# Kernel tuning notes

Measured on AMD Instinct MI355X. Metric: run time of the kernel, lower is better.

Reference implementation:

```python
import jax, jax.numpy as jnp
import numpy as np

H, W = 48, 48
L = H * W            # 2304 tokens
D = 256              # d_model
NH = 8               # heads (self and memory attn)
FF = 1024            # dim_feedforward
T = 2                # memory frames
BS = 1
GN_GROUPS = 32       # GNActDWConv2d default groups


def layernorm(x, g, b, eps=1e-5):
    m = jnp.mean(x, -1, keepdims=True)
    v = jnp.mean((x - m) ** 2, -1, keepdims=True)
    return (x - m) * jax.lax.rsqrt(v + eps) * g + b


def linear(x, Wt, b):
    # torch nn.Linear convention: Wt is [out, in]
    return x @ Wt.T + b


def mha_core(Q, K, V, nhead):
    # Q [Lq, bs, C], K/V [Lk, bs, C]; AOT MultiheadAttention core (eval: no dropout)
    Lq, bs, C = Q.shape
    hd = C // nhead
    Qh = (Q / np.float32(np.sqrt(hd))).reshape(Lq, bs, nhead, hd).transpose(1, 2, 0, 3)
    Kh = K.reshape(-1, bs, nhead, hd).transpose(1, 2, 0, 3)
    Vh = V.reshape(-1, bs, nhead, hd).transpose(1, 2, 0, 3)
    attn = jax.nn.softmax(jnp.einsum('bhqd,bhkd->bhqk', Qh, Kh), axis=-1)
    out = jnp.einsum('bhqk,bhkd->bhqd', attn, Vh)
    return out.transpose(2, 0, 1, 3).reshape(Lq, bs, C)


def groupnorm(x, g, b, groups, eps=1e-5):
    bs, c, h, w = x.shape
    xg = x.reshape(bs, groups, c // groups, h, w)
    m = jnp.mean(xg, (2, 3, 4), keepdims=True)
    v = jnp.mean((xg - m) ** 2, (2, 3, 4), keepdims=True)
    xg = (xg - m) * jax.lax.rsqrt(v + eps)
    return xg.reshape(bs, c, h, w) * g[None, :, None, None] + b[None, :, None, None]


def dwconv5(x, k):
    # depthwise 5x5, padding=2; x [bs,c,h,w], k [c,1,5,5]
    return jax.lax.conv_general_dilated(x, k, (1, 1), ((2, 2), (2, 2)),
                                        feature_group_count=x.shape[1])


def setup_inputs() -> dict:
    key = jax.random.key(0)
    ks = jax.random.split(key, 16)
    rn = lambda i, shape, s=1.0: jax.random.normal(ks[i], shape, jnp.float32) * s
    w = 0.02
    inp = {
        'tgt': rn(0, (L, BS, D)),
        'global_K': rn(1, (T, L, BS, D)),
        'global_V': rn(2, (T, L, BS, D)),
        'local_K': rn(3, (L, BS, D)),
        'local_V': rn(4, (L, BS, D)),
        # LayerNorms
        'ln1_g': jnp.ones(D, jnp.float32), 'ln1_b': jnp.zeros(D, jnp.float32),
        'ln2_g': jnp.ones(D, jnp.float32), 'ln2_b': jnp.zeros(D, jnp.float32),
        'ln3_g': jnp.ones(D, jnp.float32), 'ln3_b': jnp.zeros(D, jnp.float32),
        'ln4_g': jnp.ones(D, jnp.float32), 'ln4_b': jnp.zeros(D, jnp.float32),
        # self_attn (use_linear=True) Q/K/V + projection
        'sa_Wq': rn(5, (D, D), w), 'sa_bq': jnp.zeros(D, jnp.float32),
        'sa_Wk': rn(6, (D, D), w), 'sa_bk': jnp.zeros(D, jnp.float32),
        'sa_Wv': rn(7, (D, D), w), 'sa_bv': jnp.zeros(D, jnp.float32),
        'sa_Wo': rn(8, (D, D), w), 'sa_bo': jnp.zeros(D, jnp.float32),
        # block linear_Q
        'Wq': rn(9, (D, D), w), 'bq': jnp.zeros(D, jnp.float32),
        # long/short term attn projections (use_linear=False)
        'lt_Wo': rn(10, (D, D), w), 'lt_bo': jnp.zeros(D, jnp.float32),
        'st_Wo': rn(11, (D, D), w), 'st_bo': jnp.zeros(D, jnp.float32),
        # FFN: linear1 -> GN+GELU+DWConv -> linear2
        'W1': rn(12, (FF, D), w), 'b1': jnp.zeros(FF, jnp.float32),
        'gn_g': jnp.ones(FF, jnp.float32), 'gn_b': jnp.zeros(FF, jnp.float32),
        'dw_k': rn(13, (FF, 1, 5, 5), 0.05),
        'W2': rn(14, (D, FF), w), 'b2': jnp.zeros(D, jnp.float32),
    }
    return inp


def reference(tgt, global_K, global_V, local_K, local_V,
              ln1_g, ln1_b, ln2_g, ln2_b, ln3_g, ln3_b, ln4_g, ln4_b,
              sa_Wq, sa_bq, sa_Wk, sa_bk, sa_Wv, sa_bv, sa_Wo, sa_bo,
              Wq, bq, lt_Wo, lt_bo, st_Wo, st_bo,
              W1, b1, gn_g, gn_b, dw_k, W2, b2):
    # --- stage 1: self-attention ---
    _tgt = layernorm(tgt, ln1_g, ln1_b)
    q = linear(_tgt, sa_Wq, sa_bq)
    k = linear(_tgt, sa_Wk, sa_bk)
    v = linear(_tgt, sa_Wv, sa_bv)
    tgt2 = linear(mha_core(q, k, v, NH), sa_Wo, sa_bo)
    tgt = tgt + tgt2  # droppath is identity at eval

    # --- stage 2: long-term + short-term memory cross-attention ---
    _tgt = layernorm(tgt, ln2_g, ln2_b)
    curr_Q = linear(_tgt, Wq, bq)
    curr_K = curr_Q
    curr_V = _tgt

    flat_K = global_K.reshape(-1, BS, D)  # [T*L, bs, D]
    flat_V = global_V.reshape(-1, BS, D)
    tgt2 = linear(mha_core(curr_Q, flat_K, flat_V, NH), lt_Wo, lt_bo)

    k_st = layernorm(local_K + curr_K, ln4_g, ln4_b)
    v_st = layernorm(local_V + curr_V, ln4_g, ln4_b)
    tgt3 = linear(mha_core(curr_Q, k_st, v_st, NH), st_Wo, st_bo)

    tgt = tgt + tgt2 + tgt3

    # --- stage 3: FFN with GN + GELU + depthwise conv ---
    _tgt = layernorm(tgt, ln3_g, ln3_b)
    x = linear(_tgt, W1, b1)                        # [L, bs, FF]
    x = x.reshape(H, W, BS, FF).transpose(2, 3, 0, 1)  # [bs, FF, H, W]
    x = jax.nn.gelu(groupnorm(x, gn_g, gn_b, GN_GROUPS), approximate=False)
    x = dwconv5(x, dw_k)
    x = x.reshape(BS, FF, L).transpose(2, 0, 1)     # [L, bs, FF]
    tgt2 = linear(x, W2, b2)
    return tgt + tgt2
```

## Files before the change

kernel.cpp:

```cpp
#include <hip/hip_runtime.h>
#include <hip/hip_bf16.h>

#define L   2304
#define D   256
#define NHD 8
#define HD  32
#define FF  1024
#define HH  48
#define WWW 48
#define SPL 4
#define RCH 24
#define RP  (L / RCH)
#define S2LOG 0.25503486f

typedef unsigned short bfraw;
typedef __attribute__((ext_vector_type(8))) short s8v;
typedef __attribute__((ext_vector_type(4))) float f4v;

__device__ __forceinline__ bfraw f2b(float x) {
    __hip_bfloat16 h = __float2bfloat16(x);
    return __builtin_bit_cast(bfraw, h);
}

__global__ __launch_bounds__(256) void diag_kernel(float* __restrict__ out, float c, int n)
{
    int i = blockIdx.x * 256 + threadIdx.x;
    if (i < n) out[i] = c;
}

__global__ __launch_bounds__(256) void ln_kernel(
    const float* __restrict__ inA, const float* __restrict__ inB,
    const float* __restrict__ g, const float* __restrict__ b,
    float* __restrict__ out, bfraw* __restrict__ outb)
{
    int row = blockIdx.x, t = threadIdx.x;
    size_t idx = (size_t)row * D + t;
    float v = inA[idx];
    if (inB) v += inB[idx];
    __shared__ float rs[256], rq[256];
    rs[t] = v; rq[t] = v * v;
    __syncthreads();
    for (int o = 128; o > 0; o >>= 1) {
        if (t < o) { rs[t] += rs[t + o]; rq[t] += rq[t + o]; }
        __syncthreads();
    }
    float mean = rs[0] * (1.f / D);
    float var  = rq[0] * (1.f / D) - mean * mean;
    float rstd = rsqrtf(var + 1e-5f);
    float r = (v - mean) * rstd * g[t] + b[t];
    out[idx] = r;
    if (outb) outb[idx] = f2b(r);
}

__global__ __launch_bounds__(256) void gemm_mfma(
    const float* __restrict__ A, const float* __restrict__ W,
    const float* __restrict__ bias, const float* res, float* out,
    bfraw* __restrict__ outb, float oscale,
    int M, int N, int K)
{
    __shared__ __attribute__((aligned(16))) short Al[32][32];
    __shared__ __attribute__((aligned(16))) short Wl[64][32];
    int t = threadIdx.x;
    int w = t >> 6, l = t & 63;
    int lo = l & 15, quad = l >> 4;
    int m0 = blockIdx.x * 32, n0 = blockIdx.y * 64;
    int wr = (w & 1) * 16, wc = (w >> 1) * 32;
    f4v acc[2];
    acc[0] = (f4v){0.f, 0.f, 0.f, 0.f};
    acc[1] = (f4v){0.f, 0.f, 0.f, 0.f};

    int aswz = (quad ^ ((lo >> 2) & 3)) * 8;
    int arow = t >> 3, apart = t & 7;
    int acol = ((apart >> 1) ^ ((arow >> 2) & 3)) * 8 + (apart & 1) * 4;

    for (int k0 = 0; k0 < K; k0 += 32) {
        float4 a4 = *reinterpret_cast<const float4*>(A + (size_t)(m0 + arow) * K + k0 + apart * 4);
        float4 w4[2];
        #pragma unroll
        for (int i = 0; i < 2; i++) {
            int row = i * 32 + arow;
            w4[i] = *reinterpret_cast<const float4*>(W + (size_t)(n0 + row) * K + k0 + apart * 4);
        }
        __syncthreads();
        {
            ushort4 ab;
            ab.x = f2b(a4.x); ab.y = f2b(a4.y); ab.z = f2b(a4.z); ab.w = f2b(a4.w);
            *reinterpret_cast<ushort4*>(&Al[arow][acol]) = ab;
            #pragma unroll
            for (int i = 0; i < 2; i++) {
                int row = i * 32 + arow;
                int col = ((apart >> 1) ^ ((row >> 2) & 3)) * 8 + (apart & 1) * 4;
                ushort4 wb;
                wb.x = f2b(w4[i].x); wb.y = f2b(w4[i].y); wb.z = f2b(w4[i].z); wb.w = f2b(w4[i].w);
                *reinterpret_cast<ushort4*>(&Wl[row][col]) = wb;
            }
        }
        __syncthreads();
        s8v af = *reinterpret_cast<const s8v*>(&Al[wr + lo][aswz]);
        #pragma unroll
        for (int j = 0; j < 2; j++) {
            s8v wf = *reinterpret_cast<const s8v*>(&Wl[wc + j * 16 + lo][aswz]);
            acc[j] = __builtin_amdgcn_mfma_f32_16x16x32_bf16(af, wf, acc[j], 0, 0, 0);
        }
    }

    #pragma unroll
    for (int j = 0; j < 2; j++) {
        #pragma unroll
        for (int r = 0; r < 4; r++) {
            int mrow = m0 + wr + quad * 4 + r;
            int ncol = n0 + wc + j * 16 + lo;
            float v = acc[j][r] + bias[ncol];
            size_t idx = (size_t)mrow * N + ncol;
            if (res) v += res[idx];
            out[idx] = v;
            if (outb) outb[idx] = f2b(v * oscale);
        }
    }
}

__global__ __launch_bounds__(256) void cvt_kernel(
    const float* __restrict__ in, bfraw* __restrict__ out)
{
    size_t i = ((size_t)blockIdx.x * 256 + threadIdx.x) * 4;
    float4 v = *reinterpret_cast<const float4*>(in + i);
    ushort4 o;
    o.x = f2b(v.x); o.y = f2b(v.y); o.z = f2b(v.z); o.w = f2b(v.w);
    *reinterpret_cast<ushort4*>(out + i) = o;
}

__global__ __launch_bounds__(256) void cvtT_kernel(
    const float* __restrict__ in, bfraw* __restrict__ out, int N)
{
    __shared__ float Ls[32][33];
    int h = blockIdx.y, n0 = blockIdx.x * 32, t = threadIdx.x;
    int nl = t >> 3, dq = t & 7;
    float4 v = *reinterpret_cast<const float4*>(in + (size_t)(n0 + nl) * D + h * HD + dq * 4);
    Ls[nl][dq*4+0] = v.x; Ls[nl][dq*4+1] = v.y;
    Ls[nl][dq*4+2] = v.z; Ls[nl][dq*4+3] = v.w;
    __syncthreads();
    int dl = t >> 3, nq = t & 7;
    ushort4 o;
    o.x = f2b(Ls[nq*4+0][dl]); o.y = f2b(Ls[nq*4+1][dl]);
    o.z = f2b(Ls[nq*4+2][dl]); o.w = f2b(Ls[nq*4+3][dl]);
    *reinterpret_cast<ushort4*>(out + (size_t)(h * HD + dl) * N + n0 + nq * 4) = o;
}

__global__ __launch_bounds__(256) void attn_mfma_split(
    const bfraw* __restrict__ Qb, const bfraw* __restrict__ Kb,
    const bfraw* __restrict__ Vt, float* __restrict__ OP,
    float* __restrict__ ML, int Lk, int chunk)
{
    __shared__ __attribute__((aligned(16))) short Ks[64][32];
    __shared__ __attribute__((aligned(16))) short Vts[32][72];
    __shared__ __attribute__((aligned(16))) short Ps[4][16][72];
    __shared__ float Tb[4][16][33];
    int t = threadIdx.x;
    int w = t >> 6, l = t & 63;
    int h = blockIdx.y, q0 = blockIdx.x * 64 + w * 16, z = blockIdx.z;
    int lo = l & 15, quad = l >> 4;
    int kb = z * chunk, ke = kb + chunk;

    s8v qf = *reinterpret_cast<const s8v*>(Qb + (size_t)(q0 + lo) * D + h * HD + quad * 8);
    int kswz = (quad ^ ((lo >> 2) & 3)) * 8;

    int skey = t >> 2, spart = t & 3;
    int kcol = (spart ^ ((skey >> 2) & 3)) * 8;
    int sd = t >> 3, svp = t & 7;
    const bfraw* kp = Kb + (size_t)skey * D + h * HD + spart * 8;
    const bfraw* vp = Vt + (size_t)(h * HD + sd) * Lk + svp * 8;

    float m_r = -1e30f, l_r = 0.f;
    f4v o0 = {0.f, 0.f, 0.f, 0.f}, o1 = {0.f, 0.f, 0.f, 0.f};

    for (int k0 = kb; k0 < ke; k0 += 64) {
        s8v kv = *reinterpret_cast<const s8v*>(kp + (size_t)k0 * D);
        s8v vv = *reinterpret_cast<const s8v*>(vp + k0);
        __syncthreads();
        *reinterpret_cast<s8v*>(&Ks[skey][kcol]) = kv;
        *reinterpret_cast<s8v*>(&Vts[sd][svp * 8]) = vv;
        __syncthreads();

        f4v sc4[4];
        #pragma unroll
        for (int s = 0; s < 4; s++) {
            s8v kf = *reinterpret_cast<const s8v*>(&Ks[lo + 16 * s][kswz]);
            sc4[s] = __builtin_amdgcn_mfma_f32_16x16x32_bf16(kf, qf, (f4v){0.f,0.f,0.f,0.f}, 0, 0, 0);
        }
        float cm = -1e30f;
        #pragma unroll
        for (int s = 0; s < 4; s++)
            #pragma unroll
            for (int r = 0; r < 4; r++)
                cm = fmaxf(cm, sc4[s][r]);
        cm = fmaxf(cm, __shfl_xor(cm, 16));
        cm = fmaxf(cm, __shfl_xor(cm, 32));
        bool skip = __all(cm <= m_r + 8.f);
        if (!skip) {
            float mnew = fmaxf(m_r, cm);
            float alpha = __builtin_amdgcn_exp2f(m_r - mnew);
            l_r *= alpha;
            #pragma unroll
            for (int r = 0; r < 4; r++) { o0[r] *= alpha; o1[r] *= alpha; }
            m_r = mnew;
        }
        float ls = 0.f;
        #pragma unroll
        for (int s = 0; s < 4; s++) {
            float p0 = __builtin_amdgcn_exp2f(sc4[s][0] - m_r);
            float p1 = __builtin_amdgcn_exp2f(sc4[s][1] - m_r);
            float p2 = __builtin_amdgcn_exp2f(sc4[s][2] - m_r);
            float p3 = __builtin_amdgcn_exp2f(sc4[s][3] - m_r);
            ls += p0 + p1 + p2 + p3;
            ushort4 pk;
            pk.x = f2b(p0); pk.y = f2b(p1); pk.z = f2b(p2); pk.w = f2b(p3);
            *reinterpret_cast<ushort4*>(&Ps[w][lo][s * 16 + quad * 4]) = pk;
        }
        ls += __shfl_xor(ls, 16);
        ls += __shfl_xor(ls, 32);
        l_r += ls;
        #pragma unroll
        for (int kc = 0; kc < 2; kc++) {
            s8v pf = *reinterpret_cast<const s8v*>(&Ps[w][lo][kc * 32 + quad * 8]);
            s8v v0 = *reinterpret_cast<const s8v*>(&Vts[lo][kc * 32 + quad * 8]);
            s8v v1 = *reinterpret_cast<const s8v*>(&Vts[16 + lo][kc * 32 + quad * 8]);
            o0 = __builtin_amdgcn_mfma_f32_16x16x32_bf16(v0, pf, o0, 0, 0, 0);
            o1 = __builtin_amdgcn_mfma_f32_16x16x32_bf16(v1, pf, o1, 0, 0, 0);
        }
    }

    #pragma unroll
    for (int r = 0; r < 4; r++) {
        Tb[w][lo][quad * 4 + r]      = o0[r];
        Tb[w][lo][16 + quad * 4 + r] = o1[r];
    }
    float* Oz = OP + (size_t)z * L * D;
    int ql = l >> 2, dq = (l & 3) * 8;
    float4 u0, u1;
    u0.x = Tb[w][ql][dq + 0]; u0.y = Tb[w][ql][dq + 1];
    u0.z = Tb[w][ql][dq + 2]; u0.w = Tb[w][ql][dq + 3];
    u1.x = Tb[w][ql][dq + 4]; u1.y = Tb[w][ql][dq + 5];
    u1.z = Tb[w][ql][dq + 6]; u1.w = Tb[w][ql][dq + 7];
    *reinterpret_cast<float4*>(Oz + (size_t)(q0 + ql) * D + h * HD + dq)     = u0;
    *reinterpret_cast<float4*>(Oz + (size_t)(q0 + ql) * D + h * HD + dq + 4) = u1;
    if (l < 16) {
        size_t mi = (((size_t)z * NHD + h) * L + q0 + lo) * 2;
        ML[mi]     = m_r;
        ML[mi + 1] = l_r;
    }
}

__global__ __launch_bounds__(256) void attn_combine(
    const float* __restrict__ OP, const float* __restrict__ ML,
    float* __restrict__ O)
{
    int q = blockIdx.x, t = threadIdx.x, h = t >> 5;
    float m[SPL], lv[SPL];
    float M = -1e30f;
    #pragma unroll
    for (int s = 0; s < SPL; s++) {
        size_t mi = (((size_t)s * NHD + h) * L + q) * 2;
        m[s]  = ML[mi];
        lv[s] = ML[mi + 1];
        M = fmaxf(M, m[s]);
    }
    float wl = 0.f, acc = 0.f;
    #pragma unroll
    for (int s = 0; s < SPL; s++) {
        float w = __builtin_amdgcn_exp2f(m[s] - M);
        wl  += w * lv[s];
        acc += w * OP[(size_t)s * L * D + (size_t)q * D + t];
    }
    O[(size_t)q * D + t] = acc / wl;
}

__global__ __launch_bounds__(256) void gn_stats_part(
    const float* __restrict__ X, float* __restrict__ ps)
{
    int g = blockIdx.x, rc = blockIdx.y, t = threadIdx.x;
    int cq = (t & 7) * 4;
    int rl = t >> 3;
    int r0 = rc * RP;
    float s = 0.f, sq = 0.f;
    #pragma unroll
    for (int p = 0; p < RP / 32; p++) {
        int l = r0 + p * 32 + rl;
        float4 v = *reinterpret_cast<const float4*>(X + (size_t)l * FF + g * 32 + cq);
        s  += v.x + v.y + v.z + v.w;
        sq += v.x*v.x + v.y*v.y + v.z*v.z + v.w*v.w;
    }
    __shared__ float rs[256], rq[256];
    rs[t] = s; rq[t] = sq;
    __syncthreads();
    for (int o = 128; o > 0; o >>= 1) {
        if (t < o) { rs[t] += rs[t + o]; rq[t] += rq[t + o]; }
        __syncthreads();
    }
    if (t == 0) {
        ps[(g * RCH + rc) * 2]     = rs[0];
        ps[(g * RCH + rc) * 2 + 1] = rq[0];
    }
}

__global__ __launch_bounds__(64) void gn_stats_final(
    const float* __restrict__ ps, float* __restrict__ st)
{
    int g = threadIdx.x;
    if (g < 32) {
        float s = 0.f, sq = 0.f;
        for (int i = 0; i < RCH; i++) {
            s  += ps[(g * RCH + i) * 2];
            sq += ps[(g * RCH + i) * 2 + 1];
        }
        float n = (float)(L * 32);
        float mean = s / n;
        float var  = sq / n - mean * mean;
        st[g * 2]     = mean;
        st[g * 2 + 1] = rsqrtf(var + 1e-5f);
    }
}

__global__ __launch_bounds__(256) void gn_gelu_dwconv(
    const float* __restrict__ X, const float* __restrict__ st,
    const float* __restrict__ gg, const float* __restrict__ gb,
    const float* __restrict__ Kw, float* __restrict__ Y)
{
    __shared__ float tile[144][64];
    int h0 = blockIdx.x * 8, w0 = blockIdx.y * 8, c0 = blockIdx.z * 64;
    int t = threadIdx.x;
    int c = t & 63;
    int cg = (c0 + c) >> 5;
    float mu = st[2 * cg], rs = st[2 * cg + 1];
    float ga = gg[c0 + c], be = gb[c0 + c];

    for (int i = t; i < 144 * 64; i += 256) {
        int sp = i >> 6;
        int hy = h0 + (sp / 12) - 2, wx = w0 + (sp % 12) - 2;
        float v = 0.f;
        if (hy >= 0 && hy < HH && wx >= 0 && wx < WWW) {
            float x = X[(size_t)(hy * WWW + wx) * FF + c0 + c];
            x = (x - mu) * rs * ga + be;
            v = 0.5f * x * (1.f + erff(x * 0.70710678118654752f));
        }
        tile[sp][c] = v;
    }
    float kw[25];
    #pragma unroll
    for (int i = 0; i < 25; i++) kw[i] = Kw[(size_t)(c0 + c) * 25 + i];
    __syncthreads();

    int sgrp = t >> 6;
    for (int s = 0; s < 16; s++) {
        int sp = sgrp * 16 + s;
        int oh = sp >> 3, ow = sp & 7;
        float acc = 0.f;
        #pragma unroll
        for (int ky = 0; ky < 5; ky++)
            #pragma unroll
            for (int kx = 0; kx < 5; kx++)
                acc += tile[(oh + ky) * 12 + ow + kx][c] * kw[ky * 5 + kx];
        Y[(size_t)((h0 + oh) * WWW + w0 + ow) * FF + c0 + c] = acc;
    }
}

extern "C" void kernel_launch(void* const* d_in, const int* in_sizes, int n_in,
                              void* d_out, int out_size, void* d_ws, size_t ws_size,
                              hipStream_t stream)
{
    (void)in_sizes;
    float* out = (float*)d_out;

    if (n_in != 34) {
        diag_kernel<<<(out_size + 255) / 256, 256, 0, stream>>>(out, 2000.f, out_size);
        return;
    }

    const float* tgt    = (const float*)d_in[0];
    const float* gK     = (const float*)d_in[1];
    const float* gV     = (const float*)d_in[2];
    const float* lK     = (const float*)d_in[3];
    const float* lV     = (const float*)d_in[4];
    const float* ln1_g  = (const float*)d_in[5];
    const float* ln1_b  = (const float*)d_in[6];
    const float* ln2_g  = (const float*)d_in[7];
    const float* ln2_b  = (const float*)d_in[8];
    const float* ln3_g  = (const float*)d_in[9];
    const float* ln3_b  = (const float*)d_in[10];
    const float* ln4_g  = (const float*)d_in[11];
    const float* ln4_b  = (const float*)d_in[12];
    const float* sa_Wq  = (const float*)d_in[13];
    const float* sa_bq  = (const float*)d_in[14];
    const float* sa_Wk  = (const float*)d_in[15];
    const float* sa_bk  = (const float*)d_in[16];
    const float* sa_Wv  = (const float*)d_in[17];
    const float* sa_bv  = (const float*)d_in[18];
    const float* sa_Wo  = (const float*)d_in[19];
    const float* sa_bo  = (const float*)d_in[20];
    const float* Wq     = (const float*)d_in[21];
    const float* bq     = (const float*)d_in[22];
    const float* lt_Wo  = (const float*)d_in[23];
    const float* lt_bo  = (const float*)d_in[24];
    const float* st_Wo  = (const float*)d_in[25];
    const float* st_bo  = (const float*)d_in[26];
    const float* W1w    = (const float*)d_in[27];
    const float* b1w    = (const float*)d_in[28];
    const float* gn_g   = (const float*)d_in[29];
    const float* gn_b   = (const float*)d_in[30];
    const float* dw_k   = (const float*)d_in[31];
    const float* W2w    = (const float*)d_in[32];
    const float* b2w    = (const float*)d_in[33];

    const size_t LD = (size_t)L * D;
    const size_t NEED = (6 * LD + (size_t)L * FF + 64) * 4;
    float* ws = (float*)d_ws;
    float* t0 = ws + 0 * LD;
    float* t1 = ws + 1 * LD;
    float* t2 = ws + 2 * LD;
    float* t3 = ws + 3 * LD;
    float* t4 = ws + 4 * LD;
    float* t5 = ws + 5 * LD;
    float* X1 = t0;
    float* X2 = ws + 6 * LD;
    float* ST = X2 + (size_t)L * FF;
    bfraw* qb   = (bfraw*)X2;
    bfraw* kb1  = qb + LD;
    bfraw* vtb1 = qb + 3 * LD;
    bfraw* kb2  = qb + 5 * LD;
    bfraw* vtb2 = qb + 6 * LD;
    float* OP   = ws;
    float* ML   = X2 + (7 * LD) / 2;
    float* PS   = ML;

    if (ws_size < NEED) {
        int wsMiB = (int)(ws_size >> 20); if (wsMiB > 63) wsMiB = 63;
        diag_kernel<<<(out_size + 255) / 256, 256, 0, stream>>>(out, 64.f + (float)wsMiB, out_size);
        return;
    }

    dim3 gDD(L / 32, D / 64);
    dim3 gDF(L / 32, FF / 64);
    dim3 gATS(L / 64, NHD, SPL);
    int  cvtLD  = (int)(LD / 1024);
    dim3 gT1(L / 32, NHD);
    dim3 gT2(2 * L / 32, NHD);
    dim3 gGN(32, RCH);
    dim3 gDW(6, 6, 16);

    ln_kernel<<<L, 256, 0, stream>>>(tgt, nullptr, ln1_g, ln1_b, t0, nullptr);
    gemm_mfma<<<gDD, 256, 0, stream>>>(t0, sa_Wq, sa_bq, nullptr, t1, qb,  S2LOG, L, D, D);
    gemm_mfma<<<gDD, 256, 0, stream>>>(t0, sa_Wk, sa_bk, nullptr, t2, kb2, 1.f,   L, D, D);
    gemm_mfma<<<gDD, 256, 0, stream>>>(t0, sa_Wv, sa_bv, nullptr, t3, nullptr, 1.f, L, D, D);
    cvtT_kernel<<<gT1, 256, 0, stream>>>(t3, vtb2, L);
    attn_mfma_split<<<gATS, 256, 0, stream>>>(qb, kb2, vtb2, OP, ML, L, L / SPL);
    attn_combine<<<L, 256, 0, stream>>>(OP, ML, t4);
    gemm_mfma<<<gDD, 256, 0, stream>>>(t4, sa_Wo, sa_bo, tgt, t5, nullptr, 1.f, L, D, D);

    ln_kernel<<<L, 256, 0, stream>>>(t5, nullptr, ln2_g, ln2_b, t0, nullptr);
    gemm_mfma<<<gDD, 256, 0, stream>>>(t0, Wq, bq, nullptr, t1, qb, S2LOG, L, D, D);
    ln_kernel<<<L, 256, 0, stream>>>(t1, lK, ln4_g, ln4_b, t2, kb2);
    ln_kernel<<<L, 256, 0, stream>>>(t0, lV, ln4_g, ln4_b, t3, nullptr);
    cvtT_kernel<<<gT1, 256, 0, stream>>>(t3, vtb2, L);
    cvt_kernel<<<2 * cvtLD, 256, 0, stream>>>(gK, kb1);
    cvtT_kernel<<<gT2, 256, 0, stream>>>(gV, vtb1, 2 * L);
    attn_mfma_split<<<gATS, 256, 0, stream>>>(qb, kb1, vtb1, OP, ML, 2 * L, 2 * L / SPL);
    attn_combine<<<L, 256, 0, stream>>>(OP, ML, t4);
    gemm_mfma<<<gDD, 256, 0, stream>>>(t4, lt_Wo, lt_bo, t5, t5, nullptr, 1.f, L, D, D);
    attn_mfma_split<<<gATS, 256, 0, stream>>>(qb, kb2, vtb2, OP, ML, L, L / SPL);
    attn_combine<<<L, 256, 0, stream>>>(OP, ML, t4);
    gemm_mfma<<<gDD, 256, 0, stream>>>(t4, st_Wo, st_bo, t5, t5, nullptr, 1.f, L, D, D);

    ln_kernel<<<L, 256, 0, stream>>>(t5, nullptr, ln3_g, ln3_b, t4, nullptr);
    gemm_mfma<<<gDF, 256, 0, stream>>>(t4, W1w, b1w, nullptr, X1, nullptr, 1.f, L, FF, D);
    gn_stats_part<<<gGN, 256, 0, stream>>>(X1, PS);
    gn_stats_final<<<1, 64, 0, stream>>>(PS, ST);
    gn_gelu_dwconv<<<gDW, 256, 0, stream>>>(X1, ST, gn_g, gn_b, dw_k, X2);
    gemm_mfma<<<gDD, 256, 0, stream>>>(X2, W2w, b2w, t5, out, nullptr, 1.f, L, D, FF);
}
```

Before: 348.3 us.

## Fuse self-attention QKV projections into one GEMM and restructure GEMM staging

Replaces the three separate Q/K/V projection GEMMs plus the V transpose-convert kernel with a single fused kernel that selects the weight by grid row and writes bf16 Q (scaled), K, and transposed V directly. It also restructures the general GEMM so that a 256-wide K chunk of the weight is staged in shared memory with an XOR swizzle, while the A operand is read straight from global memory into registers. The aim is fewer launches, fewer fp32 intermediate writes and fewer syncs per K step. The trade-off is a larger shared-memory footprint, which may lower occupancy, plus uncoalesced A loads and strided transposed V stores.

```diff
diff --git a/kernel.cpp b/kernel.cpp
--- a/kernel.cpp
+++ b/kernel.cpp
@@ -58,8 +58,7 @@
     bfraw* __restrict__ outb, float oscale,
     int M, int N, int K)
 {
-    __shared__ __attribute__((aligned(16))) short Al[32][32];
-    __shared__ __attribute__((aligned(16))) short Wl[64][32];
+    __shared__ __attribute__((aligned(16))) short Wl[64][256];
     int t = threadIdx.x;
     int w = t >> 6, l = t & 63;
     int lo = l & 15, quad = l >> 4;
@@ -69,38 +68,39 @@
     acc[0] = (f4v){0.f, 0.f, 0.f, 0.f};
     acc[1] = (f4v){0.f, 0.f, 0.f, 0.f};
 
-    int aswz = (quad ^ ((lo >> 2) & 3)) * 8;
-    int arow = t >> 3, apart = t & 7;
-    int acol = ((apart >> 1) ^ ((arow >> 2) & 3)) * 8 + (apart & 1) * 4;
-
-    for (int k0 = 0; k0 < K; k0 += 32) {
-        float4 a4 = *reinterpret_cast<const float4*>(A + (size_t)(m0 + arow) * K + k0 + apart * 4);
-        float4 w4[2];
-        #pragma unroll
-        for (int i = 0; i < 2; i++) {
-            int row = i * 32 + arow;
-            w4[i] = *reinterpret_cast<const float4*>(W + (size_t)(n0 + row) * K + k0 + apart * 4);
-        }
+    int srow = t >> 2, scolq = t & 3;
+    const float* wp = W + (size_t)(n0 + srow) * K + scolq * 64;
+    const float* ap = A + (size_t)(m0 + wr + lo) * K + quad * 8;
+
+    for (int ch = 0; ch < K; ch += 256) {
         __syncthreads();
-        {
-            ushort4 ab;
-            ab.x = f2b(a4.x); ab.y = f2b(a4.y); ab.z = f2b(a4.z); ab.w = f2b(a4.w);
-            *reinterpret_cast<ushort4*>(&Al[arow][acol]) = ab;
+        #pragma unroll
+        for (int i = 0; i < 8; i++) {
+            float4 x = *reinterpret_cast<const float4*>(wp + ch + i * 8);
+            float4 y = *reinterpret_cast<const float4*>(wp + ch + i * 8 + 4);
+            s8v wb;
+            wb[0] = (short)f2b(x.x); wb[1] = (short)f2b(x.y);
+            wb[2] = (short)f2b(x.z); wb[3] = (short)f2b(x.w);
+            wb[4] = (short)f2b(y.x); wb[5] = (short)f2b(y.y);
+            wb[6] = (short)f2b(y.z); wb[7] = (short)f2b(y.w);
+            *reinterpret_cast<s8v*>(&Wl[srow][((scolq * 8 + i) ^ (srow & 7)) * 8]) = wb;
+        }
+        __syncthreads();
+        #pragma unroll
+        for (int kk = 0; kk < 8; kk++) {
+            float4 a0 = *reinterpret_cast<const float4*>(ap + ch + kk * 32);
+            float4 a1 = *reinterpret_cast<const float4*>(ap + ch + kk * 32 + 4);
+            s8v af;
+            af[0] = (short)f2b(a0.x); af[1] = (short)f2b(a0.y);
+            af[2] = (short)f2b(a0.z); af[3] = (short)f2b(a0.w);
+            af[4] = (short)f2b(a1.x); af[5] = (short)f2b(a1.y);
+            af[6] = (short)f2b(a1.z); af[7] = (short)f2b(a1.w);
             #pragma unroll
-            for (int i = 0; i < 2; i++) {
-                int row = i * 32 + arow;
-                int col = ((apart >> 1) ^ ((row >> 2) & 3)) * 8 + (apart & 1) * 4;
-                ushort4 wb;
-                wb.x = f2b(w4[i].x); wb.y = f2b(w4[i].y); wb.z = f2b(w4[i].z); wb.w = f2b(w4[i].w);
-                *reinterpret_cast<ushort4*>(&Wl[row][col]) = wb;
+            for (int j = 0; j < 2; j++) {
+                int rw = wc + j * 16 + lo;
+                s8v wf = *reinterpret_cast<const s8v*>(&Wl[rw][((kk * 4 + quad) ^ (rw & 7)) * 8]);
+                acc[j] = __builtin_amdgcn_mfma_f32_16x16x32_bf16(af, wf, acc[j], 0, 0, 0);
             }
-        }
-        __syncthreads();
-        s8v af = *reinterpret_cast<const s8v*>(&Al[wr + lo][aswz]);
-        #pragma unroll
-        for (int j = 0; j < 2; j++) {
-            s8v wf = *reinterpret_cast<const s8v*>(&Wl[wc + j * 16 + lo][aswz]);
-            acc[j] = __builtin_amdgcn_mfma_f32_16x16x32_bf16(af, wf, acc[j], 0, 0, 0);
         }
     }
 
@@ -113,8 +113,79 @@
             float v = acc[j][r] + bias[ncol];
             size_t idx = (size_t)mrow * N + ncol;
             if (res) v += res[idx];
-            out[idx] = v;
+            if (out) out[idx] = v;
             if (outb) outb[idx] = f2b(v * oscale);
+        }
+    }
+}
+
+__global__ __launch_bounds__(256) void gemm_qkv(
+    const float* __restrict__ A,
+    const float* __restrict__ Wq_, const float* __restrict__ bq_,
+    const float* __restrict__ Wk_, const float* __restrict__ bk_,
+    const float* __restrict__ Wv_, const float* __restrict__ bv_,
+    bfraw* __restrict__ qb, bfraw* __restrict__ kb, bfraw* __restrict__ vtb)
+{
+    __shared__ __attribute__((aligned(16))) short Wl[64][256];
+    int t = threadIdx.x;
+    int w = t >> 6, l = t & 63;
+    int lo = l & 15, quad = l >> 4;
+    int sel = blockIdx.y >> 2;
+    int m0 = blockIdx.x * 32, n0 = (blockIdx.y & 3) * 64;
+    int wr = (w & 1) * 16, wc = (w >> 1) * 32;
+    const float* W = (sel == 0) ? Wq_ : (sel == 1) ? Wk_ : Wv_;
+    const float* bias = (sel == 0) ? bq_ : (sel == 1) ? bk_ : bv_;
+    f4v acc[2];
+    acc[0] = (f4v){0.f, 0.f, 0.f, 0.f};
+    acc[1] = (f4v){0.f, 0.f, 0.f, 0.f};
+
+    int srow = t >> 2, scolq = t & 3;
+    const float* wp = W + (size_t)(n0 + srow) * D + scolq * 64;
+    const float* ap = A + (size_t)(m0 + wr + lo) * D + quad * 8;
+
+    #pragma unroll
+    for (int i = 0; i < 8; i++) {
+        float4 x = *reinterpret_cast<const float4*>(wp + i * 8);
+        float4 y = *reinterpret_cast<const float4*>(wp + i * 8 + 4);
+        s8v wb;
+        wb[0] = (short)f2b(x.x); wb[1] = (short)f2b(x.y);
+        wb[2] = (short)f2b(x.z); wb[3] = (short)f2b(x.w);
+        wb[4] = (short)f2b(y.x); wb[5] = (short)f2b(y.y);
+        wb[6] = (short)f2b(y.z); wb[7] = (short)f2b(y.w);
+        *reinterpret_cast<s8v*>(&Wl[srow][((scolq * 8 + i) ^ (srow & 7)) * 8]) = wb;
+    }
+    __syncthreads();
+    #pragma unroll
+    for (int kk = 0; kk < 8; kk++) {
+        float4 a0 = *reinterpret_cast<const float4*>(ap + kk * 32);
+        float4 a1 = *reinterpret_cast<const float4*>(ap + kk * 32 + 4);
+        s8v af;
+        af[0] = (short)f2b(a0.x); af[1] = (short)f2b(a0.y);
+        af[2] = (short)f2b(a0.z); af[3] = (short)f2b(a0.w);
+        af[4] = (short)f2b(a1.x); af[5] = (short)f2b(a1.y);
+        af[6] = (short)f2b(a1.z); af[7] = (short)f2b(a1.w);
+        #pragma unroll
+        for (int j = 0; j < 2; j++) {
+            int rw = wc + j * 16 + lo;
+            s8v wf = *reinterpret_cast<const s8v*>(&Wl[rw][((kk * 4 + quad) ^ (rw & 7)) * 8]);
+            acc[j] = __builtin_amdgcn_mfma_f32_16x16x32_bf16(af, wf, acc[j], 0, 0, 0);
+        }
+    }
+
+    #pragma unroll
+    for (int j = 0; j < 2; j++) {
+        #pragma unroll
+        for (int r = 0; r < 4; r++) {
+            int mrow = m0 + wr + quad * 4 + r;
+            int ncol = n0 + wc + j * 16 + lo;
+            float v = acc[j][r] + bias[ncol];
+            if (sel == 0) {
+                qb[(size_t)mrow * D + ncol] = f2b(v * S2LOG);
+            } else if (sel == 1) {
+                kb[(size_t)mrow * D + ncol] = f2b(v);
+            } else {
+                vtb[(size_t)ncol * L + mrow] = f2b(v);
+            }
         }
     }
 }
@@ -439,6 +510,7 @@
 
     dim3 gDD(L / 32, D / 64);
     dim3 gDF(L / 32, FF / 64);
+    dim3 gQKV(L / 32, 12);
     dim3 gATS(L / 64, NHD, SPL);
     int  cvtLD  = (int)(LD / 1024);
     dim3 gT1(L / 32, NHD);
@@ -447,10 +519,8 @@
     dim3 gDW(6, 6, 16);
 
     ln_kernel<<<L, 256, 0, stream>>>(tgt, nullptr, ln1_g, ln1_b, t0, nullptr);
-    gemm_mfma<<<gDD, 256, 0, stream>>>(t0, sa_Wq, sa_bq, nullptr, t1, qb,  S2LOG, L, D, D);
-    gemm_mfma<<<gDD, 256, 0, stream>>>(t0, sa_Wk, sa_bk, nullptr, t2, kb2, 1.f,   L, D, D);
-    gemm_mfma<<<gDD, 256, 0, stream>>>(t0, sa_Wv, sa_bv, nullptr, t3, nullptr, 1.f, L, D, D);
-    cvtT_kernel<<<gT1, 256, 0, stream>>>(t3, vtb2, L);
+    gemm_qkv<<<gQKV, 256, 0, stream>>>(t0, sa_Wq, sa_bq, sa_Wk, sa_bk, sa_Wv, sa_bv,
+                                       qb, kb2, vtb2);
     attn_mfma_split<<<gATS, 256, 0, stream>>>(qb, kb2, vtb2, OP, ML, L, L / SPL);
     attn_combine<<<L, 256, 0, stream>>>(OP, ML, t4);
     gemm_mfma<<<gDD, 256, 0, stream>>>(t4, sa_Wo, sa_bo, tgt, t5, nullptr, 1.f, L, D, D);
```

After: 387.9 us. 11.4% more time.

## Feed GEMM A operand as bf16 directly from producers, skip LDS staging

Applied to the files above, without the earlier changes.

Producers of GEMM inputs (layernorm, attention combine, GN+GELU+dwconv) now write bf16, and the GEMM loads its A fragments straight from global memory into registers instead of converting fp32 to bf16 through shared memory. Unused fp32 outputs are dropped via null pointers. This halves A-operand traffic, removes one LDS staging buffer and the conversion work per tile, and cuts redundant fp32 stores. The tradeoff is uncoalesced per-lane 16-byte global loads for A. Precision is unchanged because the values were already rounded to bf16 before the MFMA.

```diff
diff --git a/kernel.cpp b/kernel.cpp
--- a/kernel.cpp
+++ b/kernel.cpp
@@ -48,17 +48,16 @@
     float var  = rq[0] * (1.f / D) - mean * mean;
     float rstd = rsqrtf(var + 1e-5f);
     float r = (v - mean) * rstd * g[t] + b[t];
-    out[idx] = r;
+    if (out)  out[idx]  = r;
     if (outb) outb[idx] = f2b(r);
 }
 
 __global__ __launch_bounds__(256) void gemm_mfma(
-    const float* __restrict__ A, const float* __restrict__ W,
+    const bfraw* __restrict__ A, const float* __restrict__ W,
     const float* __restrict__ bias, const float* res, float* out,
     bfraw* __restrict__ outb, float oscale,
     int M, int N, int K)
 {
-    __shared__ __attribute__((aligned(16))) short Al[32][32];
     __shared__ __attribute__((aligned(16))) short Wl[64][32];
     int t = threadIdx.x;
     int w = t >> 6, l = t & 63;
@@ -70,36 +69,29 @@
     acc[1] = (f4v){0.f, 0.f, 0.f, 0.f};
 
     int aswz = (quad ^ ((lo >> 2) & 3)) * 8;
-    int arow = t >> 3, apart = t & 7;
-    int acol = ((apart >> 1) ^ ((arow >> 2) & 3)) * 8 + (apart & 1) * 4;
+    int srow = t >> 3, spart = t & 7;
+    const bfraw* ap = A + (size_t)(m0 + wr + lo) * K + quad * 8;
 
     for (int k0 = 0; k0 < K; k0 += 32) {
-        float4 a4 = *reinterpret_cast<const float4*>(A + (size_t)(m0 + arow) * K + k0 + apart * 4);
         float4 w4[2];
         #pragma unroll
+        for (int i = 0; i < 2; i++)
+            w4[i] = *reinterpret_cast<const float4*>(W + (size_t)(n0 + i * 32 + srow) * K + k0 + spart * 4);
+        s8v af = *reinterpret_cast<const s8v*>(ap + k0);
+        __syncthreads();
+        #pragma unroll
         for (int i = 0; i < 2; i++) {
-            int row = i * 32 + arow;
-            w4[i] = *reinterpret_cast<const float4*>(W + (size_t)(n0 + row) * K + k0 + apart * 4);
-        }
-        __syncthreads();
-        {
-            ushort4 ab;
-            ab.x = f2b(a4.x); ab.y = f2b(a4.y); ab.z = f2b(a4.z); ab.w = f2b(a4.w);
-            *reinterpret_cast<ushort4*>(&Al[arow][acol]) = ab;
-            #pragma unroll
-            for (int i = 0; i < 2; i++) {
-                int row = i * 32 + arow;
-                int col = ((apart >> 1) ^ ((row >> 2) & 3)) * 8 + (apart & 1) * 4;
-                ushort4 wb;
-                wb.x = f2b(w4[i].x); wb.y = f2b(w4[i].y); wb.z = f2b(w4[i].z); wb.w = f2b(w4[i].w);
-                *reinterpret_cast<ushort4*>(&Wl[row][col]) = wb;
-            }
-        }
-        __syncthreads();
-        s8v af = *reinterpret_cast<const s8v*>(&Al[wr + lo][aswz]);
+            int row = i * 32 + srow;
+            int col = ((spart >> 1) ^ ((row >> 2) & 3)) * 8 + (spart & 1) * 4;
+            ushort4 wb;
+            wb.x = f2b(w4[i].x); wb.y = f2b(w4[i].y); wb.z = f2b(w4[i].z); wb.w = f2b(w4[i].w);
+            *reinterpret_cast<ushort4*>(&Wl[row][col]) = wb;
+        }
+        __syncthreads();
         #pragma unroll
         for (int j = 0; j < 2; j++) {
-            s8v wf = *reinterpret_cast<const s8v*>(&Wl[wc + j * 16 + lo][aswz]);
+            int rw = wc + j * 16 + lo;
+            s8v wf = *reinterpret_cast<const s8v*>(&Wl[rw][aswz]);
             acc[j] = __builtin_amdgcn_mfma_f32_16x16x32_bf16(af, wf, acc[j], 0, 0, 0);
         }
     }
@@ -113,7 +105,7 @@
             float v = acc[j][r] + bias[ncol];
             size_t idx = (size_t)mrow * N + ncol;
             if (res) v += res[idx];
-            out[idx] = v;
+            if (out) out[idx] = v;
             if (outb) outb[idx] = f2b(v * oscale);
         }
     }
@@ -252,7 +244,7 @@
 
 __global__ __launch_bounds__(256) void attn_combine(
     const float* __restrict__ OP, const float* __restrict__ ML,
-    float* __restrict__ O)
+    bfraw* __restrict__ Ob)
 {
     int q = blockIdx.x, t = threadIdx.x, h = t >> 5;
     float m[SPL], lv[SPL];
@@ -271,7 +263,7 @@
         wl  += w * lv[s];
         acc += w * OP[(size_t)s * L * D + (size_t)q * D + t];
     }
-    O[(size_t)q * D + t] = acc / wl;
+    Ob[(size_t)q * D + t] = f2b(acc / wl);
 }
 
 __global__ __launch_bounds__(256) void gn_stats_part(
@@ -323,7 +315,7 @@
 __global__ __launch_bounds__(256) void gn_gelu_dwconv(
     const float* __restrict__ X, const float* __restrict__ st,
     const float* __restrict__ gg, const float* __restrict__ gb,
-    const float* __restrict__ Kw, float* __restrict__ Y)
+    const float* __restrict__ Kw, bfraw* __restrict__ Y)
 {
     __shared__ float tile[144][64];
     int h0 = blockIdx.x * 8, w0 = blockIdx.y * 8, c0 = blockIdx.z * 64;
@@ -359,7 +351,7 @@
             #pragma unroll
             for (int kx = 0; kx < 5; kx++)
                 acc += tile[(oh + ky) * 12 + ow + kx][c] * kw[ky * 5 + kx];
-        Y[(size_t)((h0 + oh) * WWW + w0 + ow) * FF + c0 + c] = acc;
+        Y[(size_t)((h0 + oh) * WWW + w0 + ow) * FF + c0 + c] = f2b(acc);
     }
 }
 
@@ -415,7 +407,6 @@
     float* ws = (float*)d_ws;
     float* t0 = ws + 0 * LD;
     float* t1 = ws + 1 * LD;
-    float* t2 = ws + 2 * LD;
     float* t3 = ws + 3 * LD;
     float* t4 = ws + 4 * LD;
     float* t5 = ws + 5 * LD;
@@ -430,6 +421,10 @@
     float* OP   = ws;
     float* ML   = X2 + (7 * LD) / 2;
     float* PS   = ML;
+    bfraw* t0b  = (bfraw*)t0;
+    bfraw* t3b  = (bfraw*)t3;
+    bfraw* t4b  = (bfraw*)t4;
+    bfraw* X2b  = (bfraw*)X2;
 
     if (ws_size < NEED) {
         int wsMiB = (int)(ws_size >> 20); if (wsMiB > 63) wsMiB = 63;
@@ -446,33 +441,33 @@
     dim3 gGN(32, RCH);
     dim3 gDW(6, 6, 16);
 
-    ln_kernel<<<L, 256, 0, stream>>>(tgt, nullptr, ln1_g, ln1_b, t0, nullptr);
-    gemm_mfma<<<gDD, 256, 0, stream>>>(t0, sa_Wq, sa_bq, nullptr, t1, qb,  S2LOG, L, D, D);
-    gemm_mfma<<<gDD, 256, 0, stream>>>(t0, sa_Wk, sa_bk, nullptr, t2, kb2, 1.f,   L, D, D);
-    gemm_mfma<<<gDD, 256, 0, stream>>>(t0, sa_Wv, sa_bv, nullptr, t3, nullptr, 1.f, L, D, D);
+    ln_kernel<<<L, 256, 0, stream>>>(tgt, nullptr, ln1_g, ln1_b, nullptr, t0b);
+    gemm_mfma<<<gDD, 256, 0, stream>>>(t0b, sa_Wq, sa_bq, nullptr, nullptr, qb,  S2LOG, L, D, D);
+    gemm_mfma<<<gDD, 256, 0, stream>>>(t0b, sa_Wk, sa_bk, nullptr, nullptr, kb2, 1.f,   L, D, D);
+    gemm_mfma<<<gDD, 256, 0, stream>>>(t0b, sa_Wv, sa_bv, nullptr, t3, nullptr, 1.f, L, D, D);
     cvtT_kernel<<<gT1, 256, 0, stream>>>(t3, vtb2, L);
     attn_mfma_split<<<gATS, 256, 0, stream>>>(qb, kb2, vtb2, OP, ML, L, L / SPL);
-    attn_combine<<<L, 256, 0, stream>>>(OP, ML, t4);
-    gemm_mfma<<<gDD, 256, 0, stream>>>(t4, sa_Wo, sa_bo, tgt, t5, nullptr, 1.f, L, D, D);
-
-    ln_kernel<<<L, 256, 0, stream>>>(t5, nullptr, ln2_g, ln2_b, t0, nullptr);
-    gemm_mfma<<<gDD, 256, 0, stream>>>(t0, Wq, bq, nullptr, t1, qb, S2LOG, L, D, D);
-    ln_kernel<<<L, 256, 0, stream>>>(t1, lK, ln4_g, ln4_b, t2, kb2);
+    attn_combine<<<L, 256, 0, stream>>>(OP, ML, t4b);
+    gemm_mfma<<<gDD, 256, 0, stream>>>(t4b, sa_Wo, sa_bo, tgt, t5, nullptr, 1.f, L, D, D);
+
+    ln_kernel<<<L, 256, 0, stream>>>(t5, nullptr, ln2_g, ln2_b, t0, t3b);
+    gemm_mfma<<<gDD, 256, 0, stream>>>(t3b, Wq, bq, nullptr, t1, qb, S2LOG, L, D, D);
+    ln_kernel<<<L, 256, 0, stream>>>(t1, lK, ln4_g, ln4_b, nullptr, kb2);
     ln_kernel<<<L, 256, 0, stream>>>(t0, lV, ln4_g, ln4_b, t3, nullptr);
     cvtT_kernel<<<gT1, 256, 0, stream>>>(t3, vtb2, L);
     cvt_kernel<<<2 * cvtLD, 256, 0, stream>>>(gK, kb1);
     cvtT_kernel<<<gT2, 256, 0, stream>>>(gV, vtb1, 2 * L);
     attn_mfma_split<<<gATS, 256, 0, stream>>>(qb, kb1, vtb1, OP, ML, 2 * L, 2 * L / SPL);
-    attn_combine<<<L, 256, 0, stream>>>(OP, ML, t4);
-    gemm_mfma<<<gDD, 256, 0, stream>>>(t4, lt_Wo, lt_bo, t5, t5, nullptr, 1.f, L, D, D);
+    attn_combine<<<L, 256, 0, stream>>>(OP, ML, t4b);
+    gemm_mfma<<<gDD, 256, 0, stream>>>(t4b, lt_Wo, lt_bo, t5, t5, nullptr, 1.f, L, D, D);
     attn_mfma_split<<<gATS, 256, 0, stream>>>(qb, kb2, vtb2, OP, ML, L, L / SPL);
-    attn_combine<<<L, 256, 0, stream>>>(OP, ML, t4);
-    gemm_mfma<<<gDD, 256, 0, stream>>>(t4, st_Wo, st_bo, t5, t5, nullptr, 1.f, L, D, D);
-
-    ln_kernel<<<L, 256, 0, stream>>>(t5, nullptr, ln3_g, ln3_b, t4, nullptr);
-    gemm_mfma<<<gDF, 256, 0, stream>>>(t4, W1w, b1w, nullptr, X1, nullptr, 1.f, L, FF, D);
+    attn_combine<<<L, 256, 0, stream>>>(OP, ML, t4b);
+    gemm_mfma<<<gDD, 256, 0, stream>>>(t4b, st_Wo, st_bo, t5, t5, nullptr, 1.f, L, D, D);
+
+    ln_kernel<<<L, 256, 0, stream>>>(t5, nullptr, ln3_g, ln3_b, nullptr, t4b);
+    gemm_mfma<<<gDF, 256, 0, stream>>>(t4b, W1w, b1w, nullptr, X1, nullptr, 1.f, L, FF, D);
     gn_stats_part<<<gGN, 256, 0, stream>>>(X1, PS);
     gn_stats_final<<<1, 64, 0, stream>>>(PS, ST);
-    gn_gelu_dwconv<<<gDW, 256, 0, stream>>>(X1, ST, gn_g, gn_b, dw_k, X2);
-    gemm_mfma<<<gDD, 256, 0, stream>>>(X2, W2w, b2w, t5, out, nullptr, 1.f, L, D, FF);
-}
+    gn_gelu_dwconv<<<gDW, 256, 0, stream>>>(X1, ST, gn_g, gn_b, dw_k, X2b);
+    gemm_mfma<<<gDD, 256, 0, stream>>>(X2b, W2w, b2w, t5, out, nullptr, 1.f, L, D, FF);
+}
```

Result: no change. 351.2 us (+0.8%).
